# Kernel tuning notes

Hardware: AMD Instinct MI355X
Metric: run time of the kernel (lower is better)

Reference implementation:

```python
import jax, jax.numpy as jnp
import numpy as np

Q_LATTICE = 4      # nested lattice alphabet size
QMAX_ACT = 127.0   # 2**(8-1) - 1 for 8-bit LSQ


def _lattice_quantize(x_blocks, G, Ginv, q):
    # x_blocks: [N, 8] rows are block vectors. Lattice point = z @ G, z integer.
    z = jnp.round(x_blocks @ Ginv)
    half = q // 2
    z_mod = jnp.mod(z + half, q) - half  # nested (mod-q) lattice, centered
    return z_mod @ G


def setup_inputs() -> dict:
    key = jax.random.key(0)
    k1, k2 = jax.random.split(key)
    O, I, BS = 4096, 4096, 8
    rng = np.random.default_rng(0)
    G_np = np.eye(BS, dtype=np.float64) + 0.1 * rng.standard_normal((BS, BS))
    Ginv_np = np.linalg.inv(G_np)
    return {
        "x": jax.random.normal(k1, (256, I), dtype=jnp.float32),
        "weight": jax.random.normal(k2, (O, I), dtype=jnp.float32),
        "bias": jnp.zeros((O,), dtype=jnp.float32),
        "theta_beta": jnp.ones((O, 1), dtype=jnp.float32),
        "alpha": jnp.ones((1,), dtype=jnp.float32),
        "G": jnp.asarray(G_np, dtype=jnp.float32),
        "Ginv": jnp.asarray(Ginv_np, dtype=jnp.float32),
    }


def reference(x, weight, bias, theta_beta, alpha, G, Ginv):
    O, I = weight.shape
    bs = G.shape[0]
    nblk = I // bs
    sg = jax.lax.stop_gradient

    # --- hierarchical nested-lattice weight quantization (row tiling) ---
    W_blocks = weight.reshape(O, nblk, bs)
    # theta_beta [O, k] -> mean over k -> [O, 1, 1], broadcast to all blocks
    scale_w = jnp.mean(theta_beta, axis=-1, keepdims=True)[:, None, :]
    W_scaled = (W_blocks * scale_w).reshape(-1, bs)
    # straight-through lattice quantize
    W_q = W_scaled + sg(_lattice_quantize(W_scaled, G, Ginv, Q_LATTICE) - W_scaled)
    W_q = W_q.reshape(O, I)

    # --- linear ---
    y = x @ W_q.T + bias

    # --- LSQ activation quantization ---
    a = jax.nn.relu(alpha) + 1e-8          # [1]
    y_clipped = y + sg(jnp.clip(y, -a, a) - y)  # ste_clip (clamp detached)
    s = a / QMAX_ACT
    y_scaled = y_clipped / s
    y_round = y_scaled + sg(jnp.round(y_scaled) - y_scaled)  # ste_round
    return y_round * s
```

## Files before the change

### kernel.cpp

```cpp
#include <hip/hip_runtime.h>

typedef __attribute__((ext_vector_type(8))) __bf16 bf16x8;
typedef __attribute__((ext_vector_type(4))) float f32x4;

#define M_ 256
#define N_ 4096
#define K_ 4096
#define SPLITK 4
#define KC (K_ / SPLITK)
#define BM 128
#define BN 64
#define BK 32
#define KSTEPS (KC / BK)
#define NCH 20
#define LDSBUF 20480



__device__ __forceinline__ unsigned short f2bf(float f) {
  unsigned int u = __builtin_bit_cast(unsigned int, f);
  u += 0x7fffu + ((u >> 16) & 1u);
  return (unsigned short)(u >> 16);
}

__device__ __forceinline__ void async16(const void* g, void* l) {
  __builtin_amdgcn_global_load_lds(
      (const __attribute__((address_space(1))) unsigned int*)g,
      (__attribute__((address_space(3))) unsigned int*)l, 16, 0, 0);
}

__device__ __forceinline__ float lsq1(float y, float a, float s) {
  float yc = fminf(fmaxf(y, -a), a);
  return rintf(yc / s) * s;
}

#define ZLUT 0x3F800000BF80C000ull

__device__ __forceinline__ uint4 zdec(unsigned int w) {
  unsigned int d[4];
#pragma unroll
  for (int p = 0; p < 4; ++p) {
    const unsigned int lo = (unsigned int)((ZLUT >> (((w >> (4 * p)) & 3u) * 16)) & 0xFFFFull);
    const unsigned int hi = (unsigned int)((ZLUT >> (((w >> (4 * p + 2)) & 3u) * 16)) & 0xFFFFull);
    d[p] = lo | (hi << 16);
  }
  return make_uint4(d[0], d[1], d[2], d[3]);
}


#define NQB ((N_ * K_ / 8) / 256)
#define NXB ((M_ * K_ / 8) / 256)

__global__ __launch_bounds__(256) void k_prep(const float* __restrict__ W,
                                              const float* __restrict__ theta,
                                              const float* __restrict__ Ginv,
                                              const float* __restrict__ x,
                                              const float* __restrict__ G,
                                              unsigned short* __restrict__ z2,
                                              unsigned short* __restrict__ hi,
                                              unsigned short* __restrict__ lo,
                                              int kTheta) {
  __shared__ float Ms[64];
  const int tid = threadIdx.x;
  const bool isQ = blockIdx.x < NQB;
  if (tid < 64) Ms[tid] = isQ ? Ginv[tid] : G[tid];
  __syncthreads();

  if (isQ) {
#pragma clang fp contract(off)
    const int s = blockIdx.x * 256 + tid;
    const int lane6 = s & 63;
    const int tile = s >> 6;
    const int o  = ((tile >> 7) << 4) + (lane6 & 15);
    const int kb = ((tile & 127) << 2) + (lane6 >> 4);
    const float4* wp = (const float4*)(W + ((size_t)o << 12) + ((size_t)kb << 3));
    const float4 w0 = wp[0], w1 = wp[1];
    float sc = 0.f;
    for (int t = 0; t < kTheta; ++t) sc += theta[o * kTheta + t];
    sc /= (float)kTheta;
    const float wsv[8] = {w0.x * sc, w0.y * sc, w0.z * sc, w0.w * sc,
                          w1.x * sc, w1.y * sc, w1.z * sc, w1.w * sc};
    unsigned int word = 0u;
#pragma unroll
    for (int i = 0; i < 8; ++i) {
      float t = 0.f;
#pragma unroll
      for (int j = 0; j < 8; ++j)
        t = t + wsv[j] * Ms[j * 8 + i];
      const int zi = (int)rintf(t);
      word |= (unsigned int)((zi + 2) & 3) << (2 * i);
    }
    z2[s] = (unsigned short)word;
  } else {
    const int s = (blockIdx.x - NQB) * 256 + tid;
    const int lane6 = s & 63;
    const int tile = s >> 6;
    const int m  = ((tile >> 7) << 4) + (lane6 & 15);
    const int kb = ((tile & 127) << 2) + (lane6 >> 4);
    const float4* xp = (const float4*)(x + ((size_t)m << 12) + ((size_t)kb << 3));
    const float4 a0 = xp[0], a1 = xp[1];
    float xv[8] = {a0.x, a0.y, a0.z, a0.w, a1.x, a1.y, a1.z, a1.w};
    unsigned int ph[4] = {0u, 0u, 0u, 0u}, pl[4] = {0u, 0u, 0u, 0u};
#pragma unroll
    for (int i = 0; i < 8; ++i) {
      float t = 0.f;
#pragma unroll
      for (int j = 0; j < 8; ++j) t = fmaf(xv[j], Ms[i * 8 + j], t);
      const unsigned short hb = f2bf(t);
      const float hf = __builtin_bit_cast(float, (unsigned int)hb << 16);
      const unsigned short lb = f2bf(t - hf);
      ph[i >> 1] |= ((unsigned int)hb) << ((i & 1) * 16);
      pl[i >> 1] |= ((unsigned int)lb) << ((i & 1) * 16);
    }
    *(uint4*)(hi + ((size_t)s << 3)) = make_uint4(ph[0], ph[1], ph[2], ph[3]);
    *(uint4*)(lo + ((size_t)s << 3)) = make_uint4(pl[0], pl[1], pl[2], pl[3]);
  }
}


__global__ __launch_bounds__(512, 4) void k_gemm(const unsigned short* __restrict__ xgh,
                                                 const unsigned short* __restrict__ xgl,
                                                 const unsigned short* __restrict__ z2,
                                                 float* __restrict__ part) {
  __shared__ uint4 smem4[2 * LDSBUF / 16];
  char* smem = (char*)smem4;

  const int tid = threadIdx.x;
  const int lane = tid & 63, wave = tid >> 6;
  const int wr = wave >> 1, wc = wave & 1;
  const int b = blockIdx.x;
  const int mt = b & 1;
  const int sk = (b >> 1) & 3;
  const int nt = b >> 3;
  const int k0t = sk * (KC / 32);
  const int rowa16 = mt * (BM / 16);
  const int rowb16 = nt * (BN / 16);
  const int lrow = lane & 15, lkg = lane >> 4;

  const unsigned short* asrc[2];
  int aldo[2];
#pragma unroll
  for (int ci = 0; ci < 2; ++ci) {
    const unsigned short* P = (ci == 0) ? xgh : xgl;
    asrc[ci] = P + (((size_t)((rowa16 + wave) * 128 + k0t)) << 9) + lane * 8;
    aldo[ci] = (ci * 8 + wave) * 1024;
  }
  const bool brole = (wave < 4);
  const unsigned short* zsrc = nullptr;
  int bofs = 0;
  if (brole) {
    zsrc = z2 + (((size_t)((rowb16 + wave) * 128 + k0t)) << 6) + lane;
    bofs = (16 + wave) * 1024 + lane * 16;
  }

  f32x4 acc[2][2] = {};

  unsigned int zw = 0;
#pragma unroll
  for (int ci = 0; ci < 2; ++ci) async16(asrc[ci], smem + aldo[ci]);
  if (brole) {
    zw = zsrc[0];
    *(uint4*)(smem + bofs) = zdec(zw);
    zw = zsrc[64];
  }
  __syncthreads();

  for (int ks = 0; ks < KSTEPS; ++ks) {
    const int cur = (ks & 1) * LDSBUF;
    const int nxt = LDSBUF - cur;
    if (ks + 1 < KSTEPS) {
#pragma unroll
      for (int ci = 0; ci < 2; ++ci)
        async16(asrc[ci] + (size_t)(ks + 1) * 512, smem + nxt + aldo[ci]);
      if (brole) {
        *(uint4*)(smem + nxt + bofs) = zdec(zw);
        if (ks + 2 < KSTEPS) zw = zsrc[(size_t)(ks + 2) * 64];
      }
    }

    bf16x8 bfr[2], ah[2], al[2];
#pragma unroll
    for (int nf = 0; nf < 2; ++nf)
      bfr[nf] = *(const bf16x8*)(smem + cur + (16 + wc * 2 + nf) * 1024 + lane * 16);
#pragma unroll
    for (int mf = 0; mf < 2; ++mf) {
      ah[mf] = *(const bf16x8*)(smem + cur + (wr * 2 + mf) * 1024 + lane * 16);
      al[mf] = *(const bf16x8*)(smem + cur + (8 + wr * 2 + mf) * 1024 + lane * 16);
    }
#pragma unroll
    for (int mf = 0; mf < 2; ++mf)
#pragma unroll
      for (int nf = 0; nf < 2; ++nf) {
        acc[mf][nf] = __builtin_amdgcn_mfma_f32_16x16x32_bf16(ah[mf], bfr[nf], acc[mf][nf], 0, 0, 0);
        acc[mf][nf] = __builtin_amdgcn_mfma_f32_16x16x32_bf16(al[mf], bfr[nf], acc[mf][nf], 0, 0, 0);
      }
    __syncthreads();
  }

  float* pb = part + (size_t)sk * (M_ * N_);
  const int row_a = mt * BM, row_b = nt * BN;
#pragma unroll
  for (int mf = 0; mf < 2; ++mf)
#pragma unroll
    for (int nf = 0; nf < 2; ++nf)
#pragma unroll
      for (int r = 0; r < 4; ++r) {
        const int m = row_a + wr * 32 + mf * 16 + lkg * 4 + r;
        const int n = row_b + wc * 32 + nf * 16 + lrow;
        pb[(size_t)m * N_ + n] = acc[mf][nf][r];
      }
}


__global__ __launch_bounds__(256) void k_epi(const float* __restrict__ part,
                                             const float* __restrict__ bias,
                                             const float* __restrict__ alpha,
                                             float* __restrict__ out) {
  const int i4 = blockIdx.x * 256 + threadIdx.x;
  const size_t off = (size_t)i4 * 4;
  const float4 p0 = *(const float4*)(part + off);
  const float4 p1 = *(const float4*)(part + (size_t)1 * M_ * N_ + off);
  const float4 p2 = *(const float4*)(part + (size_t)2 * M_ * N_ + off);
  const float4 p3 = *(const float4*)(part + (size_t)3 * M_ * N_ + off);
  const int n = (int)(off & (N_ - 1));
  const float4 bv = *(const float4*)(bias + n);
  const float a = fmaxf(alpha[0], 0.f) + 1e-8f;
  const float s = a / 127.0f;
  float4 o;
  o.x = lsq1(((p0.x + p1.x) + p2.x) + p3.x + bv.x, a, s);
  o.y = lsq1(((p0.y + p1.y) + p2.y) + p3.y + bv.y, a, s);
  o.z = lsq1(((p0.z + p1.z) + p2.z) + p3.z + bv.z, a, s);
  o.w = lsq1(((p0.w + p1.w) + p2.w) + p3.w + bv.w, a, s);
  *(float4*)(out + off) = o;
}


extern "C" void kernel_launch(void* const* d_in, const int* in_sizes, int n_in,
                              void* d_out, int out_size, void* d_ws, size_t ws_size,
                              hipStream_t stream) {
  const float* x     = (const float*)d_in[0];
  const float* W     = (const float*)d_in[1];
  const float* bias  = (const float*)d_in[2];
  const float* theta = (const float*)d_in[3];
  const float* alpha = (const float*)d_in[4];
  const float* G     = (const float*)d_in[5];
  const float* Ginv  = (const float*)d_in[6];
  float* out = (float*)d_out;

  const int O = in_sizes[2];
  const int kTheta = in_sizes[3] / O;

  char* ws = (char*)d_ws;
  unsigned short* xgh = (unsigned short*)ws;
  unsigned short* xgl = (unsigned short*)(ws + 2097152);
  unsigned short* z2  = (unsigned short*)(ws + 4194304);
  float* part = (float*)(ws + 8388608);
  if (ws_size < 25165824) return;

  k_prep<<<NQB + NXB, 256, 0, stream>>>(W, theta, Ginv, x, G, z2, xgh, xgl, kTheta);
  k_gemm<<<2 * SPLITK * 64, 512, 0, stream>>>(xgh, xgl, z2, part);
  k_epi<<<(M_ * N_ / 4) / 256, 256, 0, stream>>>(part, bias, alpha, out);
}
```

Baseline: 49.15 us.

## Drop LDS staging in GEMM, load fragments directly into registers with wider N tile

The GEMM kernel no longer stages A and B tiles through LDS with async global-to-LDS copies and per-step barriers. Each wave now loads its pre-swizzled bf16 A hi/lo fragments and packed 2-bit lattice codes straight from global memory into registers, prefetching one K-step ahead. The N tile doubles to 128, so each wave computes a 2x4 fragment grid and the grid is halved. The 2-bit decode now uses integer-to-float conversion plus a packed bf16 convert instruction in place of a 64-bit lookup shift. In exchange, waves in the same block load duplicate A data with no shared-memory reuse, and global latency is covered by only one step of register prefetch.

```diff
diff --git a/kernel.cpp b/kernel.cpp
--- a/kernel.cpp
+++ b/kernel.cpp
@@ -9,11 +9,9 @@
 #define SPLITK 4
 #define KC (K_ / SPLITK)
 #define BM 128
-#define BN 64
+#define BN 128
 #define BK 32
 #define KSTEPS (KC / BK)
-#define NCH 20
-#define LDSBUF 20480
 
 
 
@@ -23,28 +21,23 @@
   return (unsigned short)(u >> 16);
 }
 
-__device__ __forceinline__ void async16(const void* g, void* l) {
-  __builtin_amdgcn_global_load_lds(
-      (const __attribute__((address_space(1))) unsigned int*)g,
-      (__attribute__((address_space(3))) unsigned int*)l, 16, 0, 0);
-}
-
 __device__ __forceinline__ float lsq1(float y, float a, float s) {
   float yc = fminf(fmaxf(y, -a), a);
   return rintf(yc / s) * s;
 }
 
-#define ZLUT 0x3F800000BF80C000ull
-
-__device__ __forceinline__ uint4 zdec(unsigned int w) {
-  unsigned int d[4];
-#pragma unroll
-  for (int p = 0; p < 4; ++p) {
-    const unsigned int lo = (unsigned int)((ZLUT >> (((w >> (4 * p)) & 3u) * 16)) & 0xFFFFull);
-    const unsigned int hi = (unsigned int)((ZLUT >> (((w >> (4 * p + 2)) & 3u) * 16)) & 0xFFFFull);
-    d[p] = lo | (hi << 16);
-  }
-  return make_uint4(d[0], d[1], d[2], d[3]);
+__device__ __forceinline__ bf16x8 zdec_pk(unsigned int w) {
+  unsigned int d0, d1, d2, d3;
+#define ZP(P, D)                                                        \
+  {                                                                     \
+    const float f0 = (float)((w >> (4 * P)) & 3u) - 2.0f;               \
+    const float f1 = (float)((w >> (4 * P + 2)) & 3u) - 2.0f;           \
+    asm("v_cvt_pk_bf16_f32 %0, %1, %2" : "=v"(D) : "v"(f0), "v"(f1));   \
+  }
+  ZP(0, d0) ZP(1, d1) ZP(2, d2) ZP(3, d3)
+#undef ZP
+  const uint4 u = make_uint4(d0, d1, d2, d3);
+  return __builtin_bit_cast(bf16x8, u);
 }
 
 
@@ -118,13 +111,10 @@
 }
 
 
-__global__ __launch_bounds__(512, 4) void k_gemm(const unsigned short* __restrict__ xgh,
-                                                 const unsigned short* __restrict__ xgl,
-                                                 const unsigned short* __restrict__ z2,
-                                                 float* __restrict__ part) {
-  __shared__ uint4 smem4[2 * LDSBUF / 16];
-  char* smem = (char*)smem4;
-
+__global__ __launch_bounds__(512) void k_gemm(const unsigned short* __restrict__ xgh,
+                                              const unsigned short* __restrict__ xgl,
+                                              const unsigned short* __restrict__ z2,
+                                              float* __restrict__ part) {
   const int tid = threadIdx.x;
   const int lane = tid & 63, wave = tid >> 6;
   const int wr = wave >> 1, wc = wave & 1;
@@ -133,80 +123,78 @@
   const int sk = (b >> 1) & 3;
   const int nt = b >> 3;
   const int k0t = sk * (KC / 32);
-  const int rowa16 = mt * (BM / 16);
-  const int rowb16 = nt * (BN / 16);
   const int lrow = lane & 15, lkg = lane >> 4;
 
-  const unsigned short* asrc[2];
-  int aldo[2];
-#pragma unroll
-  for (int ci = 0; ci < 2; ++ci) {
-    const unsigned short* P = (ci == 0) ? xgh : xgl;
-    asrc[ci] = P + (((size_t)((rowa16 + wave) * 128 + k0t)) << 9) + lane * 8;
-    aldo[ci] = (ci * 8 + wave) * 1024;
-  }
-  const bool brole = (wave < 4);
-  const unsigned short* zsrc = nullptr;
-  int bofs = 0;
-  if (brole) {
-    zsrc = z2 + (((size_t)((rowb16 + wave) * 128 + k0t)) << 6) + lane;
-    bofs = (16 + wave) * 1024 + lane * 16;
-  }
-
-  f32x4 acc[2][2] = {};
-
-  unsigned int zw = 0;
-#pragma unroll
-  for (int ci = 0; ci < 2; ++ci) async16(asrc[ci], smem + aldo[ci]);
-  if (brole) {
-    zw = zsrc[0];
-    *(uint4*)(smem + bofs) = zdec(zw);
-    zw = zsrc[64];
-  }
-  __syncthreads();
+  const unsigned short* ab[2];
+  const unsigned short* lb2[2];
+#pragma unroll
+  for (int mf = 0; mf < 2; ++mf) {
+    const size_t t = (size_t)((mt * 8 + wr * 2 + mf) * 128 + k0t);
+    ab[mf]  = xgh + (t << 9) + lane * 8;
+    lb2[mf] = xgl + (t << 9) + lane * 8;
+  }
+  const unsigned short* zb[4];
+#pragma unroll
+  for (int nf = 0; nf < 4; ++nf)
+    zb[nf] = z2 + (((size_t)((nt * 8 + wc * 4 + nf) * 128 + k0t)) << 6) + lane;
+
+  f32x4 acc[2][4] = {};
+
+  bf16x8 cah[2], cal[2];
+  unsigned int czw[4];
+#pragma unroll
+  for (int mf = 0; mf < 2; ++mf) {
+    cah[mf] = *(const bf16x8*)(ab[mf]);
+    cal[mf] = *(const bf16x8*)(lb2[mf]);
+  }
+#pragma unroll
+  for (int nf = 0; nf < 4; ++nf) czw[nf] = zb[nf][0];
 
   for (int ks = 0; ks < KSTEPS; ++ks) {
-    const int cur = (ks & 1) * LDSBUF;
-    const int nxt = LDSBUF - cur;
+    bf16x8 nah[2], nal[2];
+    unsigned int nzw[4];
     if (ks + 1 < KSTEPS) {
 #pragma unroll
-      for (int ci = 0; ci < 2; ++ci)
-        async16(asrc[ci] + (size_t)(ks + 1) * 512, smem + nxt + aldo[ci]);
-      if (brole) {
-        *(uint4*)(smem + nxt + bofs) = zdec(zw);
-        if (ks + 2 < KSTEPS) zw = zsrc[(size_t)(ks + 2) * 64];
+      for (int mf = 0; mf < 2; ++mf) {
+        nah[mf] = *(const bf16x8*)(ab[mf] + (size_t)(ks + 1) * 512);
+        nal[mf] = *(const bf16x8*)(lb2[mf] + (size_t)(ks + 1) * 512);
       }
+#pragma unroll
+      for (int nf = 0; nf < 4; ++nf) nzw[nf] = zb[nf][(size_t)(ks + 1) * 64];
+    } else {
+#pragma unroll
+      for (int mf = 0; mf < 2; ++mf) { nah[mf] = cah[mf]; nal[mf] = cal[mf]; }
+#pragma unroll
+      for (int nf = 0; nf < 4; ++nf) nzw[nf] = czw[nf];
     }
 
-    bf16x8 bfr[2], ah[2], al[2];
-#pragma unroll
-    for (int nf = 0; nf < 2; ++nf)
-      bfr[nf] = *(const bf16x8*)(smem + cur + (16 + wc * 2 + nf) * 1024 + lane * 16);
-#pragma unroll
-    for (int mf = 0; mf < 2; ++mf) {
-      ah[mf] = *(const bf16x8*)(smem + cur + (wr * 2 + mf) * 1024 + lane * 16);
-      al[mf] = *(const bf16x8*)(smem + cur + (8 + wr * 2 + mf) * 1024 + lane * 16);
-    }
+    bf16x8 bfr[4];
+#pragma unroll
+    for (int nf = 0; nf < 4; ++nf) bfr[nf] = zdec_pk(czw[nf]);
+
 #pragma unroll
     for (int mf = 0; mf < 2; ++mf)
 #pragma unroll
-      for (int nf = 0; nf < 2; ++nf) {
-        acc[mf][nf] = __builtin_amdgcn_mfma_f32_16x16x32_bf16(ah[mf], bfr[nf], acc[mf][nf], 0, 0, 0);
-        acc[mf][nf] = __builtin_amdgcn_mfma_f32_16x16x32_bf16(al[mf], bfr[nf], acc[mf][nf], 0, 0, 0);
+      for (int nf = 0; nf < 4; ++nf) {
+        acc[mf][nf] = __builtin_amdgcn_mfma_f32_16x16x32_bf16(cah[mf], bfr[nf], acc[mf][nf], 0, 0, 0);
+        acc[mf][nf] = __builtin_amdgcn_mfma_f32_16x16x32_bf16(cal[mf], bfr[nf], acc[mf][nf], 0, 0, 0);
       }
-    __syncthreads();
+
+#pragma unroll
+    for (int mf = 0; mf < 2; ++mf) { cah[mf] = nah[mf]; cal[mf] = nal[mf]; }
+#pragma unroll
+    for (int nf = 0; nf < 4; ++nf) czw[nf] = nzw[nf];
   }
 
   float* pb = part + (size_t)sk * (M_ * N_);
-  const int row_a = mt * BM, row_b = nt * BN;
 #pragma unroll
   for (int mf = 0; mf < 2; ++mf)
 #pragma unroll
-    for (int nf = 0; nf < 2; ++nf)
+    for (int nf = 0; nf < 4; ++nf)
 #pragma unroll
       for (int r = 0; r < 4; ++r) {
-        const int m = row_a + wr * 32 + mf * 16 + lkg * 4 + r;
-        const int n = row_b + wc * 32 + nf * 16 + lrow;
+        const int m = mt * BM + wr * 32 + mf * 16 + lkg * 4 + r;
+        const int n = nt * BN + wc * 64 + nf * 16 + lrow;
         pb[(size_t)m * N_ + n] = acc[mf][nf][r];
       }
 }
@@ -258,6 +246,6 @@
   if (ws_size < 25165824) return;
 
   k_prep<<<NQB + NXB, 256, 0, stream>>>(W, theta, Ginv, x, G, z2, xgh, xgl, kTheta);
-  k_gemm<<<2 * SPLITK * 64, 512, 0, stream>>>(xgh, xgl, z2, part);
+  k_gemm<<<2 * SPLITK * 32, 512, 0, stream>>>(xgh, xgl, z2, part);
   k_epi<<<(M_ * N_ / 4) / 256, 256, 0, stream>>>(part, bias, alpha, out);
 }
```

Measured after the change: 49.69 us. About the same (+1.1%).

## Cover full M per block so each weight tile is decoded once

Applied to the files above, without the earlier changes.

The GEMM block tile grows from 128 to the full 256 rows of M. Each block now handles one N tile and one split-K slice, and every wave covers 32 rows against all 64 columns. This halves the number of blocks and removes the duplicated z2 load and decode of the weight tile across the two M tiles. In exchange each block uses more LDS and more accumulator registers, and fewer blocks run (256 instead of 512), which may leave CUs underused on MI355X.

```diff
diff --git a/kernel.cpp b/kernel.cpp
--- a/kernel.cpp
+++ b/kernel.cpp
@@ -8,12 +8,12 @@
 #define K_ 4096
 #define SPLITK 4
 #define KC (K_ / SPLITK)
-#define BM 128
+#define BM 256
 #define BN 64
 #define BK 32
 #define KSTEPS (KC / BK)
-#define NCH 20
-#define LDSBUF 20480
+#define NCH 36
+#define LDSBUF 36864
 
 
 
@@ -118,7 +118,7 @@
 }
 
 
-__global__ __launch_bounds__(512, 4) void k_gemm(const unsigned short* __restrict__ xgh,
+__global__ __launch_bounds__(512, 2) void k_gemm(const unsigned short* __restrict__ xgh,
                                                  const unsigned short* __restrict__ xgl,
                                                  const unsigned short* __restrict__ z2,
                                                  float* __restrict__ part) {
@@ -127,37 +127,35 @@
 
   const int tid = threadIdx.x;
   const int lane = tid & 63, wave = tid >> 6;
-  const int wr = wave >> 1, wc = wave & 1;
   const int b = blockIdx.x;
-  const int mt = b & 1;
-  const int sk = (b >> 1) & 3;
-  const int nt = b >> 3;
+  const int sk = b & 3;
+  const int nt = b >> 2;
   const int k0t = sk * (KC / 32);
-  const int rowa16 = mt * (BM / 16);
-  const int rowb16 = nt * (BN / 16);
   const int lrow = lane & 15, lkg = lane >> 4;
 
-  const unsigned short* asrc[2];
-  int aldo[2];
-#pragma unroll
-  for (int ci = 0; ci < 2; ++ci) {
-    const unsigned short* P = (ci == 0) ? xgh : xgl;
-    asrc[ci] = P + (((size_t)((rowa16 + wave) * 128 + k0t)) << 9) + lane * 8;
-    aldo[ci] = (ci * 8 + wave) * 1024;
+  const unsigned short* asrc[4];
+  int aldo[4];
+#pragma unroll
+  for (int ci = 0; ci < 4; ++ci) {
+    const int c = wave * 4 + ci;
+    const unsigned short* P = (c < 16) ? xgh : xgl;
+    const int rt = c & 15;
+    asrc[ci] = P + (((size_t)(rt * 128 + k0t)) << 9) + lane * 8;
+    aldo[ci] = c * 1024;
   }
   const bool brole = (wave < 4);
   const unsigned short* zsrc = nullptr;
   int bofs = 0;
   if (brole) {
-    zsrc = z2 + (((size_t)((rowb16 + wave) * 128 + k0t)) << 6) + lane;
-    bofs = (16 + wave) * 1024 + lane * 16;
-  }
-
-  f32x4 acc[2][2] = {};
+    zsrc = z2 + (((size_t)((nt * 4 + wave) * 128 + k0t)) << 6) + lane;
+    bofs = (32 + wave) * 1024 + lane * 16;
+  }
+
+  f32x4 acc[2][4] = {};
 
   unsigned int zw = 0;
 #pragma unroll
-  for (int ci = 0; ci < 2; ++ci) async16(asrc[ci], smem + aldo[ci]);
+  for (int ci = 0; ci < 4; ++ci) async16(asrc[ci], smem + aldo[ci]);
   if (brole) {
     zw = zsrc[0];
     *(uint4*)(smem + bofs) = zdec(zw);
@@ -170,7 +168,7 @@
     const int nxt = LDSBUF - cur;
     if (ks + 1 < KSTEPS) {
 #pragma unroll
-      for (int ci = 0; ci < 2; ++ci)
+      for (int ci = 0; ci < 4; ++ci)
         async16(asrc[ci] + (size_t)(ks + 1) * 512, smem + nxt + aldo[ci]);
       if (brole) {
         *(uint4*)(smem + nxt + bofs) = zdec(zw);
@@ -178,19 +176,20 @@
       }
     }
 
-    bf16x8 bfr[2], ah[2], al[2];
-#pragma unroll
-    for (int nf = 0; nf < 2; ++nf)
-      bfr[nf] = *(const bf16x8*)(smem + cur + (16 + wc * 2 + nf) * 1024 + lane * 16);
+    bf16x8 ah[2], al[2], bfr[4];
 #pragma unroll
     for (int mf = 0; mf < 2; ++mf) {
-      ah[mf] = *(const bf16x8*)(smem + cur + (wr * 2 + mf) * 1024 + lane * 16);
-      al[mf] = *(const bf16x8*)(smem + cur + (8 + wr * 2 + mf) * 1024 + lane * 16);
-    }
+      ah[mf] = *(const bf16x8*)(smem + cur + (wave * 2 + mf) * 1024 + lane * 16);
+      al[mf] = *(const bf16x8*)(smem + cur + 16384 + (wave * 2 + mf) * 1024 + lane * 16);
+    }
+#pragma unroll
+    for (int nf = 0; nf < 4; ++nf)
+      bfr[nf] = *(const bf16x8*)(smem + cur + 32768 + nf * 1024 + lane * 16);
+
 #pragma unroll
     for (int mf = 0; mf < 2; ++mf)
 #pragma unroll
-      for (int nf = 0; nf < 2; ++nf) {
+      for (int nf = 0; nf < 4; ++nf) {
         acc[mf][nf] = __builtin_amdgcn_mfma_f32_16x16x32_bf16(ah[mf], bfr[nf], acc[mf][nf], 0, 0, 0);
         acc[mf][nf] = __builtin_amdgcn_mfma_f32_16x16x32_bf16(al[mf], bfr[nf], acc[mf][nf], 0, 0, 0);
       }
@@ -198,15 +197,14 @@
   }
 
   float* pb = part + (size_t)sk * (M_ * N_);
-  const int row_a = mt * BM, row_b = nt * BN;
 #pragma unroll
   for (int mf = 0; mf < 2; ++mf)
 #pragma unroll
-    for (int nf = 0; nf < 2; ++nf)
+    for (int nf = 0; nf < 4; ++nf)
 #pragma unroll
       for (int r = 0; r < 4; ++r) {
-        const int m = row_a + wr * 32 + mf * 16 + lkg * 4 + r;
-        const int n = row_b + wc * 32 + nf * 16 + lrow;
+        const int m = wave * 32 + mf * 16 + lkg * 4 + r;
+        const int n = nt * BN + nf * 16 + lrow;
         pb[(size_t)m * N_ + n] = acc[mf][nf][r];
       }
 }
@@ -258,6 +256,6 @@
   if (ws_size < 25165824) return;
 
   k_prep<<<NQB + NXB, 256, 0, stream>>>(W, theta, Ginv, x, G, z2, xgh, xgl, kTheta);
-  k_gemm<<<2 * SPLITK * 64, 512, 0, stream>>>(xgh, xgl, z2, part);
+  k_gemm<<<SPLITK * (N_ / BN), 512, 0, stream>>>(xgh, xgl, z2, part);
   k_epi<<<(M_ * N_ / 4) / 256, 256, 0, stream>>>(part, bias, alpha, out);
 }
```

After: 52.46 us. 6.7% more time.
